# Kernel optimization log

Hardware: AMD Instinct MI355X
Metric: run time of the kernel (lower is better)

## Reference

```python
import jax, jax.numpy as jnp
import numpy as np

N = 50000      # nodes
E = 625000     # edges
D_IN = 128     # in_feats
D_OUT = 128    # out_feats


def setup_inputs() -> dict:
    key = jax.random.key(0)
    k1, k2, k3, k4, k5, k6 = jax.random.split(key, 6)
    feat = jax.random.normal(k1, (N, D_IN), dtype=jnp.float32)
    affine = jax.random.uniform(k2, (E,), dtype=jnp.float32)
    src = jax.random.randint(k3, (E,), 0, N, dtype=jnp.int32)
    dst = jnp.sort(jax.random.randint(k4, (E,), 0, N, dtype=jnp.int32))
    # Linear(in_feats*2, out_feats): torch stores weight [out, in]; use [in, out] here
    bound = 1.0 / np.sqrt(2 * D_IN)
    W = jax.random.uniform(k5, (2 * D_IN, D_OUT), minval=-bound, maxval=bound, dtype=jnp.float32)
    b = jax.random.uniform(k6, (D_OUT,), minval=-bound, maxval=bound, dtype=jnp.float32)
    return {"feat": feat, "affine": affine, "src": src, "dst": dst, "W": W, "b": b}


def reference(feat, affine, src, dst, W, b):
    # u_mul_e: per-edge message = srcfeat[src] * edge scalar 'affine'
    msg = feat[src] * affine[:, None]                      # [E, D_IN]
    # fn.sum: scatter-add messages to destination nodes
    agg = jax.ops.segment_sum(msg, dst, num_segments=N)    # [N, D_IN]
    # concat dst features with aggregated neighborhood, then linear
    gcn_feat = jnp.concatenate([feat, agg], axis=-1)       # [N, 2*D_IN]
    return gcn_feat @ W + b                                # [N, D_OUT]
```

## Files before the change

### kernel.cpp

```cpp
#include <hip/hip_runtime.h>

#define N_NODES 50000
#define E_EDGES 625000
#define D 128

typedef __attribute__((ext_vector_type(8)))  short  short8;
typedef __attribute__((ext_vector_type(16))) float  floatx16;

static __device__ inline unsigned short f2bf(float f) {
    union { float f; unsigned u; } v; v.f = f;
    unsigned r = v.u + 0x7FFFu + ((v.u >> 16) & 1u);
    return (unsigned short)(r >> 16);
}
static __device__ inline float bflo(unsigned p) { return __uint_as_float(p << 16); }
static __device__ inline float bfhi(unsigned p) { return __uint_as_float(p & 0xFFFF0000u); }

__global__ __launch_bounds__(256) void prep_kernel(const int* __restrict__ dst,
                                                   const float* __restrict__ W,
                                                   const int* __restrict__ src,
                                                   const float* __restrict__ affine,
                                                   int* __restrict__ rowptr,
                                                   unsigned short* __restrict__ wimg,
                                                   uint2* __restrict__ meta) {
    int t = blockIdx.x * 256 + threadIdx.x;
    if (t <= N_NODES) {
        int lo = 0, hi = E_EDGES;
        while (lo < hi) {
            int mid = (lo + hi) >> 1;
            if (dst[mid] < t) lo = mid + 1; else hi = mid;
        }
        rowptr[t] = lo;
    }
    if (t < 4096) {
        int n = t & 127;
        int c = (t >> 7) & 15;
        int h = t >> 11;
        int krow = h * 128 + c * 8;
        short8 v;
        #pragma unroll
        for (int j = 0; j < 8; ++j)
            v[j] = (short)f2bf(W[(size_t)(krow + j) * D + n]);
        *((short8*)wimg + t) = v;
    }
    if (t < E_EDGES) {
        uint2 m;
        m.x = (unsigned)src[t];
        m.y = __float_as_uint(affine[t]);
        meta[t] = m;
    }
}

#define NB_M 391

__global__ __launch_bounds__(256, 3) void gemm_mfma(const float* __restrict__ feat,
                                                    const unsigned short* __restrict__ wimg,
                                                    const float* __restrict__ bias,
                                                    float* __restrict__ out,
                                                    unsigned short* __restrict__ Y) {
    __shared__ short8 Bls[2048];

    int tid = threadIdx.x;
    int idx = blockIdx.x;
    int h   = (idx >> 3) & 1;
    int b   = ((idx >> 4) << 3) | (idx & 7);
    if (b >= NB_M) return;

    const short8* wsrc = (const short8*)wimg + h * 2048;
    #pragma unroll
    for (int i = 0; i < 8; ++i)
        Bls[tid + i * 256] = wsrc[tid + i * 256];

    int wave = tid >> 6;
    int lane = tid & 63;
    int m = lane & 31;
    int g = lane >> 5;
    int row0   = b * 128 + wave * 32;
    int row_a  = row0 + m;
    int rclamp = row_a < N_NODES ? row_a : 0;

    short8 fa[8];
    const float* ap = feat + (size_t)rclamp * D + g * 8;
    #pragma unroll
    for (int ks = 0; ks < 8; ++ks) {
        float4 u = *(const float4*)(ap + ks * 16);
        float4 v = *(const float4*)(ap + ks * 16 + 4);
        short8 a;
        a[0] = (short)f2bf(u.x); a[1] = (short)f2bf(u.y);
        a[2] = (short)f2bf(u.z); a[3] = (short)f2bf(u.w);
        a[4] = (short)f2bf(v.x); a[5] = (short)f2bf(v.y);
        a[6] = (short)f2bf(v.z); a[7] = (short)f2bf(v.w);
        fa[ks] = a;
    }
    __syncthreads();

    #pragma unroll
    for (int t4 = 0; t4 < 4; ++t4) {
        int n = t4 * 32 + m;
        floatx16 acc = {0,0,0,0, 0,0,0,0, 0,0,0,0, 0,0,0,0};
        #pragma unroll
        for (int ks = 0; ks < 8; ++ks) {
            short8 bb = Bls[(ks * 2 + g) * 128 + n];
            acc = __builtin_amdgcn_mfma_f32_32x32x16_bf16(fa[ks], bb, acc, 0, 0, 0);
        }
        if (h == 0) {
            float bv = bias[n];
            #pragma unroll
            for (int r = 0; r < 16; ++r) {
                int row = row0 + (r & 3) + 8 * (r >> 2) + 4 * g;
                if (row < N_NODES) out[(size_t)row * D + n] = acc[r] + bv;
            }
        } else {
            #pragma unroll
            for (int r = 0; r < 16; ++r) {
                int row = row0 + (r & 3) + 8 * (r >> 2) + 4 * g;
                if (row < N_NODES) Y[(size_t)row * D + n] = f2bf(acc[r]);
            }
        }
    }
}

__global__ __launch_bounds__(256) void agg_add(const unsigned short* __restrict__ Y,
                                               const uint2* __restrict__ meta,
                                               const int* __restrict__ rowptr,
                                               float* __restrict__ out) {
    int wave = threadIdx.x >> 6;
    int lane = threadIdx.x & 63;
    int n = blockIdx.x * 4 + wave;
    if (n >= N_NODES) return;
    int lo = rowptr[n], hi = rowptr[n + 1];
    int g  = lane >> 4;
    int jj = (lane & 15) << 3;
    const unsigned short* Yj = Y + jj;

    float acc[8] = {0,0,0,0,0,0,0,0};

    for (int e0 = lo; e0 < hi; e0 += 16) {
        uint2 md[4];
        #pragma unroll
        for (int u = 0; u < 4; ++u) {
            int i = e0 + u * 4 + g;
            md[u] = meta[i < hi ? i : lo];
        }
        float w[4];
        uint4 p[4];
        #pragma unroll
        for (int u = 0; u < 4; ++u) {
            int i = e0 + u * 4 + g;
            w[u] = (i < hi) ? __uint_as_float(md[u].y) : 0.f;
            p[u] = *(const uint4*)(Yj + (size_t)md[u].x * D);
        }
        #pragma unroll
        for (int u = 0; u < 4; ++u) {
            acc[0] += bflo(p[u].x) * w[u];  acc[1] += bfhi(p[u].x) * w[u];
            acc[2] += bflo(p[u].y) * w[u];  acc[3] += bfhi(p[u].y) * w[u];
            acc[4] += bflo(p[u].z) * w[u];  acc[5] += bfhi(p[u].z) * w[u];
            acc[6] += bflo(p[u].w) * w[u];  acc[7] += bfhi(p[u].w) * w[u];
        }
    }

    #pragma unroll
    for (int r = 0; r < 8; ++r) {
        acc[r] += __shfl_xor(acc[r], 16);
        acc[r] += __shfl_xor(acc[r], 32);
    }

    if (g == 0) {
        float* op = out + (size_t)n * D + jj;
        float4 z0 = *(const float4*)op;
        float4 z1 = *(const float4*)(op + 4);
        z0.x += acc[0]; z0.y += acc[1]; z0.z += acc[2]; z0.w += acc[3];
        z1.x += acc[4]; z1.y += acc[5]; z1.z += acc[6]; z1.w += acc[7];
        *(float4*)op       = z0;
        *(float4*)(op + 4) = z1;
    }
}

extern "C" void kernel_launch(void* const* d_in, const int* in_sizes, int n_in,
                              void* d_out, int out_size, void* d_ws, size_t ws_size,
                              hipStream_t stream) {
    const float* feat   = (const float*)d_in[0];
    const float* affine = (const float*)d_in[1];
    const int*   src    = (const int*)  d_in[2];
    const int*   dst    = (const int*)  d_in[3];
    const float* W      = (const float*)d_in[4];
    const float* bias   = (const float*)d_in[5];
    float*       out    = (float*)d_out;

    unsigned short* wimg   = (unsigned short*)d_ws;
    int*            rowptr = (int*)((char*)d_ws + 65536);
    uint2*          meta   = (uint2*)((char*)d_ws + 266240);
    unsigned short* Y      = (unsigned short*)((char*)d_ws + 5267456);

    prep_kernel<<<(E_EDGES + 255) / 256, 256, 0, stream>>>(dst, W, src, affine,
                                                           rowptr, wimg, meta);
    int gemm_blocks = ((2 * NB_M + 15) / 16) * 16;
    gemm_mfma<<<gemm_blocks, 256, 0, stream>>>(feat, wimg, bias, out, Y);
    agg_add<<<(N_NODES + 3) / 4, 256, 0, stream>>>(Y, meta, rowptr, out);
}
```

Measured before the change: 135.4 us.

## Build rowptr by edge boundary scan and store self-term GEMM output as bf16

Rowptr is now built by having each edge thread compare its dst with the previous one and fill the rowptr entries in between. This replaces a per-node binary search over the full edge array. The self-feature half of the GEMM now writes a bf16 intermediate instead of fp32 into out, and the aggregation kernel adds bias and writes out once rather than reading and rewriting it. Together these cut global memory traffic, at the cost of rounding the self term to bf16 before it is added.

```diff
diff --git a/kernel.cpp b/kernel.cpp
--- a/kernel.cpp
+++ b/kernel.cpp
@@ -23,13 +23,16 @@
                                                    unsigned short* __restrict__ wimg,
                                                    uint2* __restrict__ meta) {
     int t = blockIdx.x * 256 + threadIdx.x;
-    if (t <= N_NODES) {
-        int lo = 0, hi = E_EDGES;
-        while (lo < hi) {
-            int mid = (lo + hi) >> 1;
-            if (dst[mid] < t) lo = mid + 1; else hi = mid;
-        }
-        rowptr[t] = lo;
+    if (t < E_EDGES) {
+        int d1 = dst[t];
+        int d0 = (t == 0) ? -1 : dst[t - 1];
+        for (int n = d0 + 1; n <= d1; ++n) rowptr[n] = t;
+        if (t == E_EDGES - 1)
+            for (int n = d1 + 1; n <= N_NODES; ++n) rowptr[n] = E_EDGES;
+        uint2 m;
+        m.x = (unsigned)src[t];
+        m.y = __float_as_uint(affine[t]);
+        meta[t] = m;
     }
     if (t < 4096) {
         int n = t & 127;
@@ -42,20 +45,13 @@
             v[j] = (short)f2bf(W[(size_t)(krow + j) * D + n]);
         *((short8*)wimg + t) = v;
     }
-    if (t < E_EDGES) {
-        uint2 m;
-        m.x = (unsigned)src[t];
-        m.y = __float_as_uint(affine[t]);
-        meta[t] = m;
-    }
 }
 
 #define NB_M 391
 
 __global__ __launch_bounds__(256, 3) void gemm_mfma(const float* __restrict__ feat,
                                                     const unsigned short* __restrict__ wimg,
-                                                    const float* __restrict__ bias,
-                                                    float* __restrict__ out,
+                                                    unsigned short* __restrict__ Z1b,
                                                     unsigned short* __restrict__ Y) {
     __shared__ short8 Bls[2048];
 
@@ -93,6 +89,8 @@
     }
     __syncthreads();
 
+    unsigned short* dstbuf = h ? Y : Z1b;
+
     #pragma unroll
     for (int t4 = 0; t4 < 4; ++t4) {
         int n = t4 * 32 + m;
@@ -102,26 +100,19 @@
             short8 bb = Bls[(ks * 2 + g) * 128 + n];
             acc = __builtin_amdgcn_mfma_f32_32x32x16_bf16(fa[ks], bb, acc, 0, 0, 0);
         }
-        if (h == 0) {
-            float bv = bias[n];
-            #pragma unroll
-            for (int r = 0; r < 16; ++r) {
-                int row = row0 + (r & 3) + 8 * (r >> 2) + 4 * g;
-                if (row < N_NODES) out[(size_t)row * D + n] = acc[r] + bv;
-            }
-        } else {
-            #pragma unroll
-            for (int r = 0; r < 16; ++r) {
-                int row = row0 + (r & 3) + 8 * (r >> 2) + 4 * g;
-                if (row < N_NODES) Y[(size_t)row * D + n] = f2bf(acc[r]);
-            }
+        #pragma unroll
+        for (int r = 0; r < 16; ++r) {
+            int row = row0 + (r & 3) + 8 * (r >> 2) + 4 * g;
+            if (row < N_NODES) dstbuf[(size_t)row * D + n] = f2bf(acc[r]);
         }
     }
 }
 
 __global__ __launch_bounds__(256) void agg_add(const unsigned short* __restrict__ Y,
+                                               const unsigned short* __restrict__ Z1b,
                                                const uint2* __restrict__ meta,
                                                const int* __restrict__ rowptr,
+                                               const float* __restrict__ bias,
                                                float* __restrict__ out) {
     int wave = threadIdx.x >> 6;
     int lane = threadIdx.x & 63;
@@ -165,13 +156,17 @@
     }
 
     if (g == 0) {
+        uint4  z  = *(const uint4*)(Z1b + (size_t)n * D + jj);
+        float4 b0 = *(const float4*)(bias + jj);
+        float4 b1 = *(const float4*)(bias + jj + 4);
         float* op = out + (size_t)n * D + jj;
-        float4 z0 = *(const float4*)op;
-        float4 z1 = *(const float4*)(op + 4);
-        z0.x += acc[0]; z0.y += acc[1]; z0.z += acc[2]; z0.w += acc[3];
-        z1.x += acc[4]; z1.y += acc[5]; z1.z += acc[6]; z1.w += acc[7];
-        *(float4*)op       = z0;
-        *(float4*)(op + 4) = z1;
+        float4 o0, o1;
+        o0.x = bflo(z.x) + b0.x + acc[0];  o0.y = bfhi(z.x) + b0.y + acc[1];
+        o0.z = bflo(z.y) + b0.z + acc[2];  o0.w = bfhi(z.y) + b0.w + acc[3];
+        o1.x = bflo(z.z) + b1.x + acc[4];  o1.y = bfhi(z.z) + b1.y + acc[5];
+        o1.z = bflo(z.w) + b1.z + acc[6];  o1.w = bfhi(z.w) + b1.w + acc[7];
+        *(float4*)op       = o0;
+        *(float4*)(op + 4) = o1;
     }
 }
 
@@ -190,10 +185,11 @@
     int*            rowptr = (int*)((char*)d_ws + 65536);
     uint2*          meta   = (uint2*)((char*)d_ws + 266240);
     unsigned short* Y      = (unsigned short*)((char*)d_ws + 5267456);
+    unsigned short* Z1b    = (unsigned short*)((char*)d_ws + 18067456);
 
     prep_kernel<<<(E_EDGES + 255) / 256, 256, 0, stream>>>(dst, W, src, affine,
                                                            rowptr, wimg, meta);
     int gemm_blocks = ((2 * NB_M + 15) / 16) * 16;
-    gemm_mfma<<<gemm_blocks, 256, 0, stream>>>(feat, wimg, bias, out, Y);
-    agg_add<<<(N_NODES + 3) / 4, 256, 0, stream>>>(Y, meta, rowptr, out);
+    gemm_mfma<<<gemm_blocks, 256, 0, stream>>>(feat, wimg, Z1b, Y);
+    agg_add<<<(N_NODES + 3) / 4, 256, 0, stream>>>(Y, Z1b, meta, rowptr, bias, out);
 }
```

After: 127.8 us. 1.06x faster.
